# Kernel optimization log

Measured on AMD Instinct MI355X. Metric: run time of the kernel, lower is better.

The kernel has to match this reference:

```python
import jax, jax.numpy as jnp
import numpy as np

N_NODES = 25000
N_EDGES = 400000
N_GRAPHS = 1000
HID = 185
IN_CH = 9
EPS = 1e-5  # BatchNorm eps (eval mode: uses running stats)


def setup_inputs() -> dict:
    key = jax.random.key(0)
    ks = jax.random.split(key, 12)
    x = jax.random.normal(ks[0], (N_NODES, IN_CH), jnp.float32)
    edge_index = jax.random.randint(ks[1], (2, N_EDGES), 0, N_NODES, jnp.int32)
    batch = jnp.sort(jax.random.randint(ks[2], (N_NODES,), 0, N_GRAPHS, jnp.int32))
    W0 = jax.random.normal(ks[3], (IN_CH, HID), jnp.float32) * 0.3
    b0 = jnp.zeros((HID,), jnp.float32)
    W_h = jax.random.normal(ks[4], (3, HID, HID), jnp.float32) * 0.07
    b_h = jnp.zeros((3, HID), jnp.float32)
    bn_gamma = 1.0 + 0.1 * jax.random.normal(ks[5], (4, HID), jnp.float32)
    bn_beta = 0.1 * jax.random.normal(ks[6], (4, HID), jnp.float32)
    bn_mean = 0.1 * jax.random.normal(ks[7], (4, HID), jnp.float32)
    bn_var = jax.random.uniform(ks[8], (4, HID), jnp.float32, 0.5, 1.5)
    W_jk = jax.random.normal(ks[9], (4 * HID, HID), jnp.float32) * 0.05
    b_jk = jnp.zeros((HID,), jnp.float32)
    W_out = jax.random.normal(ks[10], (HID, 1), jnp.float32) * 0.1
    b_out = jnp.zeros((1,), jnp.float32)
    return dict(x=x, edge_index=edge_index, batch=batch, W0=W0, b0=b0,
                W_h=W_h, b_h=b_h, bn_gamma=bn_gamma, bn_beta=bn_beta,
                bn_mean=bn_mean, bn_var=bn_var, W_jk=W_jk, b_jk=b_jk,
                W_out=W_out, b_out=b_out)


def reference(x, edge_index, batch, W0, b0, W_h, b_h, bn_gamma, bn_beta,
              bn_mean, bn_var, W_jk, b_jk, W_out, b_out):
    N = x.shape[0]
    # GCN normalization with self-loops (gcn_norm, edge_weight = 1)
    loop = jnp.arange(N, dtype=edge_index.dtype)
    src = jnp.concatenate([edge_index[0], loop])  # [E+N]
    dst = jnp.concatenate([edge_index[1], loop])  # [E+N]
    deg = jax.ops.segment_sum(jnp.ones_like(dst, dtype=x.dtype), dst, num_segments=N)
    dis = jnp.where(deg > 0, jax.lax.rsqrt(jnp.maximum(deg, 1.0)), 0.0)
    enorm = dis[src] * dis[dst]  # [E+N]

    def gcn_conv(h, W, b):
        h = h @ W                                   # [N, HID]
        msg = h[src] * enorm[:, None]               # gather + scale, [E+N, HID]
        return jax.ops.segment_sum(msg, dst, num_segments=N) + b

    def bn_relu(h, i):
        h = (h - bn_mean[i]) * jax.lax.rsqrt(bn_var[i] + EPS) * bn_gamma[i] + bn_beta[i]
        return jax.nn.relu(h)  # dropout is identity in eval mode

    xs = []
    h = bn_relu(gcn_conv(x, W0, b0), 0)
    xs.append(h)
    for i in range(3):
        h = bn_relu(gcn_conv(h, W_h[i], b_h[i]), i + 1)
        xs.append(h)
    # JumpingKnowledge 'cat' + internal lin (740 -> 185)
    h = jnp.concatenate(xs, axis=-1) @ W_jk + b_jk  # [N, HID]
    # global_max_pool over graphs
    pooled = jax.ops.segment_max(h, batch, num_segments=N_GRAPHS)  # [G, HID]
    return pooled @ W_out + b_out  # [G, 1]
```

## Files before the change

kernel.cpp:

```cpp
#include <hip/hip_runtime.h>
#include <hip/hip_bf16.h>

#define N_NODES 25000
#define N_EDGES 400000
#define N_GRAPHS 1000
#define HID 185
#define EPS 1e-5f
#define XPITCH 768
#define APITCH 36

typedef __attribute__((ext_vector_type(8))) short bf16x8;
typedef __attribute__((ext_vector_type(4))) float f32x4;

__device__ __forceinline__ short f2bf(float f) {
    union { float f; unsigned u; } v; v.f = f;
    unsigned r = v.u + 0x7FFFu + ((v.u >> 16) & 1u);
    return (short)(r >> 16);
}
__device__ __forceinline__ float bfl(unsigned u) { return __uint_as_float(u << 16); }
__device__ __forceinline__ float bfh(unsigned u) { return __uint_as_float(u & 0xFFFF0000u); }
__device__ __forceinline__ unsigned pk2(float lo, float hi) {
    return (unsigned)(unsigned short)f2bf(lo) | ((unsigned)(unsigned short)f2bf(hi) << 16);
}

#define HW (3 * 192 * 192)
#define JW (192 * 768)
#define CNTPAD 25024
__global__ void k_setup(const float* __restrict__ W_h, const float* __restrict__ W_jk,
                        const float* __restrict__ b0, const float* __restrict__ b_h,
                        const float* __restrict__ gamma, const float* __restrict__ beta,
                        const float* __restrict__ mean, const float* __restrict__ var,
                        int* __restrict__ cnt,
                        short* __restrict__ Wt_h, short* __restrict__ Wt_jk,
                        float* __restrict__ bnsc, float* __restrict__ bnsh) {
    int idx = blockIdx.x * 256 + threadIdx.x;
    if (idx < CNTPAD) { cnt[idx] = 0; return; }
    int p = idx - CNTPAD;
    if (p < HW) {
        int l = p / (192 * 192);
        int r = p % (192 * 192);
        int n = r / 192, k = r % 192;
        float v = (n < HID && k < HID) ? W_h[(l * HID + k) * HID + n] : 0.0f;
        Wt_h[p] = f2bf(v);
    } else if (p < HW + JW) {
        int j2 = p - HW;
        int n = j2 / 768, kk = j2 % 768;
        int l = kk / 192, j = kk % 192;
        float v = (n < HID && j < HID) ? W_jk[(l * HID + j) * HID + n] : 0.0f;
        Wt_jk[j2] = f2bf(v);
    } else if (p < HW + JW + 4 * 192) {
        int li = p - HW - JW;
        int l = li / 192, c = li % 192;
        float sc = 0.0f, sh = 0.0f;
        if (c < HID) {
            float bb = (l == 0) ? b0[c] : b_h[(l - 1) * HID + c];
            sc = rsqrtf(var[l * HID + c] + EPS) * gamma[l * HID + c];
            sh = (bb - mean[l * HID + c]) * sc + beta[l * HID + c];
        }
        bnsc[li] = sc;
        bnsh[li] = sh;
    }
}

__global__ void k_deg(const int* __restrict__ dst, int* cnt, int E) {
    int i = blockIdx.x * blockDim.x + threadIdx.x;
    if (i < E) atomicAdd(&cnt[dst[i]], 1);
}

__global__ __launch_bounds__(256) void k_scan(const int* __restrict__ cnt,
                                              int* __restrict__ rowptr,
                                              float* __restrict__ dis, int N) {
    __shared__ int s[256];
    const int t = threadIdx.x;
    const int b = blockIdx.x;
    int partial = 0;
    for (int i = t; i < b * 256; i += 256) partial += cnt[i];
    s[t] = partial; __syncthreads();
    for (int off = 128; off; off >>= 1) {
        if (t < off) s[t] += s[t + off];
        __syncthreads();
    }
    const int base = s[0];
    __syncthreads();
    int i = b * 256 + t;
    int v = (i < N) ? cnt[i] : 0;
    if (i < N) dis[i] = rsqrtf((float)(v + 1));
    s[t] = v; __syncthreads();
    for (int off = 1; off < 256; off <<= 1) {
        int x2 = (t >= off) ? s[t - off] : 0;
        __syncthreads();
        s[t] += x2;
        __syncthreads();
    }
    if (i < N) rowptr[i] = base + s[t] - v;
}

__global__ void k_scatter(const int* __restrict__ src, const int* __restrict__ dst,
                          const float* __restrict__ dis,
                          int* rowptr, int2* __restrict__ csr, int E) {
    int e = blockIdx.x * blockDim.x + threadIdx.x;
    if (e < E) {
        int d = dst[e];
        int s = src[e];
        int o = atomicAdd(&rowptr[d], 1);
        csr[o] = make_int2(s, __float_as_int(dis[s]));
    }
}

__global__ void k_aggr0(const float* __restrict__ x, const float* __restrict__ dis,
                        const int* __restrict__ rowptr, const int2* __restrict__ csr,
                        float* __restrict__ xa, int N) {
    int idx = blockIdx.x * blockDim.x + threadIdx.x;
    int n = idx >> 4;
    int c = idx & 15;
    if (n >= N || c >= 9) return;
    float dn = dis[n];
    float acc = x[n * 9 + c] * dn;
    int end = rowptr[n];
    int e = n ? rowptr[n - 1] : 0;
    for (; e + 4 <= end; e += 4) {
        int2 p0 = csr[e], p1 = csr[e + 1], p2 = csr[e + 2], p3 = csr[e + 3];
        acc += x[p0.x * 9 + c] * __int_as_float(p0.y)
             + x[p1.x * 9 + c] * __int_as_float(p1.y)
             + x[p2.x * 9 + c] * __int_as_float(p2.y)
             + x[p3.x * 9 + c] * __int_as_float(p3.y);
    }
    for (; e < end; ++e) {
        int2 p = csr[e];
        acc += x[p.x * 9 + c] * __int_as_float(p.y);
    }
    xa[n * 9 + c] = acc * dn;
}

__global__ __launch_bounds__(192) void k_gemm0(const float* __restrict__ A,
                                               const float* __restrict__ W,
                                               const float* __restrict__ bnsc,
                                               const float* __restrict__ bnsh,
                                               short* __restrict__ xcat, int N) {
    __shared__ float As[8 * 9];
    const int tid = threadIdx.x;
    const int r0 = blockIdx.x * 8;
    for (int idx = tid; idx < 72; idx += 192) {
        int r = idx & 7, k = idx >> 3;
        int row = r0 + r;
        As[idx] = (row < N) ? A[row * 9 + k] : 0.0f;
    }
    __syncthreads();
    const int c = tid;
    float res[8];
    #pragma unroll
    for (int r = 0; r < 8; ++r) res[r] = 0.0f;
    if (c < HID) {
        float acc[8] = {0,0,0,0,0,0,0,0};
        for (int k = 0; k < 9; ++k) {
            float w = W[k * HID + c];
            #pragma unroll
            for (int r = 0; r < 8; ++r) acc[r] += As[k * 8 + r] * w;
        }
        float sc = bnsc[c], sh = bnsh[c];
        #pragma unroll
        for (int r = 0; r < 8; ++r)
            res[r] = fmaxf(acc[r] * sc + sh, 0.0f);
    }
    #pragma unroll
    for (int r = 0; r < 8; ++r) {
        int row = r0 + r;
        if (row < N) xcat[row * XPITCH + c] = (c < HID) ? f2bf(res[r]) : (short)0;
    }
}

__global__ __launch_bounds__(192) void k_aggr(const short* __restrict__ feat, int fpitch,
                                              const float* __restrict__ dis,
                                              const int* __restrict__ rowptr,
                                              const int2* __restrict__ csr,
                                              short* __restrict__ outp, int N) {
    const int t = threadIdx.x;
    const int n = blockIdx.x * 4 + t / 48;
    const int c0 = (t % 48) * 4;
    if (n >= N) return;
    float dn = dis[n];
    float a0, a1, a2, a3;
    {
        uint2 v = *(const uint2*)(feat + (size_t)n * fpitch + c0);
        a0 = bfl(v.x) * dn; a1 = bfh(v.x) * dn; a2 = bfl(v.y) * dn; a3 = bfh(v.y) * dn;
    }
    int end = rowptr[n];
    int e = n ? rowptr[n - 1] : 0;
    for (; e + 4 <= end; e += 4) {
        int2 p0 = csr[e], p1 = csr[e + 1], p2 = csr[e + 2], p3 = csr[e + 3];
        float w0 = __int_as_float(p0.y), w1 = __int_as_float(p1.y);
        float w2 = __int_as_float(p2.y), w3 = __int_as_float(p3.y);
        uint2 v0 = *(const uint2*)(feat + (size_t)p0.x * fpitch + c0);
        uint2 v1 = *(const uint2*)(feat + (size_t)p1.x * fpitch + c0);
        uint2 v2 = *(const uint2*)(feat + (size_t)p2.x * fpitch + c0);
        uint2 v3 = *(const uint2*)(feat + (size_t)p3.x * fpitch + c0);
        a0 += bfl(v0.x) * w0; a1 += bfh(v0.x) * w0; a2 += bfl(v0.y) * w0; a3 += bfh(v0.y) * w0;
        a0 += bfl(v1.x) * w1; a1 += bfh(v1.x) * w1; a2 += bfl(v1.y) * w1; a3 += bfh(v1.y) * w1;
        a0 += bfl(v2.x) * w2; a1 += bfh(v2.x) * w2; a2 += bfl(v2.y) * w2; a3 += bfh(v2.y) * w2;
        a0 += bfl(v3.x) * w3; a1 += bfh(v3.x) * w3; a2 += bfl(v3.y) * w3; a3 += bfh(v3.y) * w3;
    }
    for (; e < end; ++e) {
        int2 p = csr[e];
        float w = __int_as_float(p.y);
        uint2 v = *(const uint2*)(feat + (size_t)p.x * fpitch + c0);
        a0 += bfl(v.x) * w; a1 += bfh(v.x) * w; a2 += bfl(v.y) * w; a3 += bfh(v.y) * w;
    }
    uint2 p;
    p.x = pk2(a0 * dn, a1 * dn);
    p.y = pk2(a2 * dn, a3 * dn);
    *(uint2*)(outp + (size_t)n * 192 + c0) = p;
}

template<int KCH, bool BNOUT>
__global__ __launch_bounds__(256) void k_mgemm(const short* __restrict__ A, int apitch,
                                               const short* __restrict__ Bt,
                                               const float* __restrict__ bnsc,
                                               const float* __restrict__ bnsh,
                                               short* __restrict__ Cout, int cpitch, int N) {
    __shared__ short As[64 * APITCH];
    __shared__ short Bs[192 * APITCH];
    const int tid = threadIdx.x;
    const int wave = tid >> 6;
    const int lane = tid & 63;
    const int quad = lane >> 4;
    const int lm = lane & 15;
    const int r0 = blockIdx.x * 64;
    const int KTOT = KCH * 32;
    const int arow = tid >> 2, aseg = tid & 3;

    f32x4 acc[4][3];
    #pragma unroll
    for (int i = 0; i < 4; ++i)
        #pragma unroll
        for (int j = 0; j < 3; ++j) acc[i][j] = (f32x4){0.f, 0.f, 0.f, 0.f};

    for (int kc = 0; kc < KCH; ++kc) {
        const int k0 = kc * 32;
        {
            int grow = r0 + arow;
            bf16x8 v = (bf16x8){0,0,0,0,0,0,0,0};
            if (grow < N) v = *(const bf16x8*)(A + (size_t)grow * apitch + k0 + aseg * 8);
            *(bf16x8*)(As + arow * APITCH + aseg * 8) = v;
        }
        #pragma unroll
        for (int i = 0; i < 3; ++i) {
            int u = tid + i * 256;
            int n = u >> 2, seg = u & 3;
            bf16x8 v = *(const bf16x8*)(Bt + n * KTOT + k0 + seg * 8);
            *(bf16x8*)(Bs + n * APITCH + seg * 8) = v;
        }
        __syncthreads();
        bf16x8 a[4], b[3];
        #pragma unroll
        for (int mt = 0; mt < 4; ++mt)
            a[mt] = *(const bf16x8*)(As + (mt * 16 + lm) * APITCH + quad * 8);
        #pragma unroll
        for (int nt = 0; nt < 3; ++nt)
            b[nt] = *(const bf16x8*)(Bs + (wave * 48 + nt * 16 + lm) * APITCH + quad * 8);
        #pragma unroll
        for (int mt = 0; mt < 4; ++mt)
            #pragma unroll
            for (int nt = 0; nt < 3; ++nt)
                acc[mt][nt] = __builtin_amdgcn_mfma_f32_16x16x32_bf16(a[mt], b[nt], acc[mt][nt], 0, 0, 0);
        __syncthreads();
    }
    #pragma unroll
    for (int nt = 0; nt < 3; ++nt) {
        int col = wave * 48 + nt * 16 + lm;
        float sc = 1.0f, sh = 0.0f;
        if (BNOUT) { sc = bnsc[col]; sh = bnsh[col]; }
        #pragma unroll
        for (int mt = 0; mt < 4; ++mt) {
            #pragma unroll
            for (int r = 0; r < 4; ++r) {
                int row = r0 + mt * 16 + quad * 4 + r;
                if (row < N) {
                    float v = acc[mt][nt][r];
                    if (BNOUT) v = fmaxf(v * sc + sh, 0.0f);
                    Cout[(size_t)row * cpitch + col] = f2bf(v);
                }
            }
        }
    }
}

__global__ __launch_bounds__(192) void k_pool_out(const short* __restrict__ jk,
                                                  const int* __restrict__ batch,
                                                  const float* __restrict__ b_jk,
                                                  const float* __restrict__ W_out,
                                                  const float* __restrict__ b_out,
                                                  float* __restrict__ out, int N) {
    __shared__ int bounds[2];
    __shared__ float partial[3];
    const int g = blockIdx.x;
    const int tid = threadIdx.x;
    if (tid < 2) {
        int key = g + tid;
        int lo = 0, hi = N;
        while (lo < hi) {
            int mid = (lo + hi) >> 1;
            if (batch[mid] < key) lo = mid + 1; else hi = mid;
        }
        bounds[tid] = lo;
    }
    __syncthreads();
    const int beg = bounds[0], end = bounds[1];
    float mx = -3.4e38f;
    for (int n = beg; n < end; ++n)
        mx = fmaxf(mx, bfl((unsigned)(unsigned short)jk[(size_t)n * 192 + tid]));
    float p = (tid < HID) ? (mx + b_jk[tid]) * W_out[tid] : 0.0f;
    #pragma unroll
    for (int off = 32; off; off >>= 1) p += __shfl_down(p, off);
    if ((tid & 63) == 0) partial[tid >> 6] = p;
    __syncthreads();
    if (tid == 0) out[g] = partial[0] + partial[1] + partial[2] + b_out[0];
}

extern "C" void kernel_launch(void* const* d_in, const int* in_sizes, int n_in,
                              void* d_out, int out_size, void* d_ws, size_t ws_size,
                              hipStream_t stream) {
    const float* x      = (const float*)d_in[0];
    const int*   ei     = (const int*)  d_in[1];
    const int*   batch  = (const int*)  d_in[2];
    const float* W0     = (const float*)d_in[3];
    const float* b0     = (const float*)d_in[4];
    const float* W_h    = (const float*)d_in[5];
    const float* b_h    = (const float*)d_in[6];
    const float* gamma  = (const float*)d_in[7];
    const float* beta   = (const float*)d_in[8];
    const float* mean   = (const float*)d_in[9];
    const float* var    = (const float*)d_in[10];
    const float* W_jk   = (const float*)d_in[11];
    const float* b_jk   = (const float*)d_in[12];
    const float* W_out  = (const float*)d_in[13];
    const float* b_out  = (const float*)d_in[14];
    float* out = (float*)d_out;

    const int N = N_NODES, E = N_EDGES, G = N_GRAPHS;
    const int NB = (N + 255) / 256;

    float* dis   = (float*)d_ws;
    float* xa    = dis + 25024;
    float* bnsc  = xa + 225024;
    float* bnsh  = bnsc + 768;
    int2*  csr   = (int2*)(bnsh + 768);
    short* xcat  = (short*)(csr + 400000);
    short* tmp16 = xcat + 19200000;
    short* Wt_h  = tmp16 + 4800000;
    short* Wt_jk = Wt_h + 110592;
    int* rowptr  = (int*)(Wt_jk + 147456);
    int* cnt     = rowptr + 25024;

    const int* src = ei;
    const int* dst = ei + E;

    k_setup<<<(CNTPAD + HW + JW + 4 * 192 + 255) / 256, 256, 0, stream>>>(
        W_h, W_jk, b0, b_h, gamma, beta, mean, var, cnt, Wt_h, Wt_jk, bnsc, bnsh);
    k_deg<<<(E + 255) / 256, 256, 0, stream>>>(dst, cnt, E);
    k_scan<<<NB, 256, 0, stream>>>(cnt, rowptr, dis, N);
    k_scatter<<<(E + 255) / 256, 256, 0, stream>>>(src, dst, dis, rowptr, csr, E);

    k_aggr0<<<(N * 16 + 255) / 256, 256, 0, stream>>>(x, dis, rowptr, csr, xa, N);
    k_gemm0<<<(N + 7) / 8, 192, 0, stream>>>(xa, W0, bnsc, bnsh, xcat, N);

    const int MB = (N + 63) / 64;
    for (int l = 1; l < 4; ++l) {
        k_aggr<<<(N + 3) / 4, 192, 0, stream>>>(xcat + (l - 1) * 192, XPITCH,
                                                dis, rowptr, csr, tmp16, N);
        k_mgemm<6, true><<<MB, 256, 0, stream>>>(tmp16, 192,
                                                 Wt_h + (l - 1) * 192 * 192,
                                                 bnsc + l * 192, bnsh + l * 192,
                                                 xcat + l * 192, XPITCH, N);
    }

    k_mgemm<24, false><<<MB, 256, 0, stream>>>(xcat, XPITCH, Wt_jk,
                                               nullptr, nullptr, tmp16, 192, N);

    k_pool_out<<<G, 192, 0, stream>>>(tmp16, batch, b_jk, W_out, b_out, out, N);
}
```

Measured before the change: 313.8 us.

## Fuse neighbor aggregation into hidden-layer GEMM kernel via shared-memory A tile

Replaces the separate aggregation kernel and BN-fused GEMM for the three hidden layers with one kernel that gathers neighbor features for a 64-row tile directly into shared memory, then runs the MFMA GEMM with BN+ReLU epilogue. This removes the intermediate tmp16 round trip through global memory and one launch per layer. In exchange, each thread now handles a whole node's 48 columns with 48 float accumulators, so the gather is less parallel (64 rows per 256-thread block, 391 blocks) and register pressure rises, which can reduce latency hiding for the irregular gathers.

```diff
diff --git a/kernel.cpp b/kernel.cpp
--- a/kernel.cpp
+++ b/kernel.cpp
@@ -169,53 +169,115 @@
     }
 }
 
-__global__ __launch_bounds__(192) void k_aggr(const short* __restrict__ feat, int fpitch,
-                                              const float* __restrict__ dis,
-                                              const int* __restrict__ rowptr,
-                                              const int2* __restrict__ csr,
-                                              short* __restrict__ outp, int N) {
-    const int t = threadIdx.x;
-    const int n = blockIdx.x * 4 + t / 48;
-    const int c0 = (t % 48) * 4;
-    if (n >= N) return;
-    float dn = dis[n];
-    float a0, a1, a2, a3;
-    {
-        uint2 v = *(const uint2*)(feat + (size_t)n * fpitch + c0);
-        a0 = bfl(v.x) * dn; a1 = bfh(v.x) * dn; a2 = bfl(v.y) * dn; a3 = bfh(v.y) * dn;
-    }
-    int end = rowptr[n];
-    int e = n ? rowptr[n - 1] : 0;
-    for (; e + 4 <= end; e += 4) {
-        int2 p0 = csr[e], p1 = csr[e + 1], p2 = csr[e + 2], p3 = csr[e + 3];
-        float w0 = __int_as_float(p0.y), w1 = __int_as_float(p1.y);
-        float w2 = __int_as_float(p2.y), w3 = __int_as_float(p3.y);
-        uint2 v0 = *(const uint2*)(feat + (size_t)p0.x * fpitch + c0);
-        uint2 v1 = *(const uint2*)(feat + (size_t)p1.x * fpitch + c0);
-        uint2 v2 = *(const uint2*)(feat + (size_t)p2.x * fpitch + c0);
-        uint2 v3 = *(const uint2*)(feat + (size_t)p3.x * fpitch + c0);
-        a0 += bfl(v0.x) * w0; a1 += bfh(v0.x) * w0; a2 += bfl(v0.y) * w0; a3 += bfh(v0.y) * w0;
-        a0 += bfl(v1.x) * w1; a1 += bfh(v1.x) * w1; a2 += bfl(v1.y) * w1; a3 += bfh(v1.y) * w1;
-        a0 += bfl(v2.x) * w2; a1 += bfh(v2.x) * w2; a2 += bfl(v2.y) * w2; a3 += bfh(v2.y) * w2;
-        a0 += bfl(v3.x) * w3; a1 += bfh(v3.x) * w3; a2 += bfl(v3.y) * w3; a3 += bfh(v3.y) * w3;
-    }
-    for (; e < end; ++e) {
-        int2 p = csr[e];
-        float w = __int_as_float(p.y);
-        uint2 v = *(const uint2*)(feat + (size_t)p.x * fpitch + c0);
-        a0 += bfl(v.x) * w; a1 += bfh(v.x) * w; a2 += bfl(v.y) * w; a3 += bfh(v.y) * w;
-    }
-    uint2 p;
-    p.x = pk2(a0 * dn, a1 * dn);
-    p.y = pk2(a2 * dn, a3 * dn);
-    *(uint2*)(outp + (size_t)n * 192 + c0) = p;
-}
-
-template<int KCH, bool BNOUT>
-__global__ __launch_bounds__(256) void k_mgemm(const short* __restrict__ A, int apitch,
+__global__ __launch_bounds__(256) void k_layer(const short* __restrict__ feat,
+                                               const float* __restrict__ dis,
+                                               const int* __restrict__ rowptr,
+                                               const int2* __restrict__ csr,
                                                const short* __restrict__ Bt,
                                                const float* __restrict__ bnsc,
                                                const float* __restrict__ bnsh,
+                                               short* __restrict__ outp, int N) {
+    __shared__ short As[6 * 64 * APITCH];
+    __shared__ short Bs[192 * APITCH];
+    const int tid = threadIdx.x;
+    const int r0 = blockIdx.x * 64;
+
+    {
+        const int r = tid >> 2;
+        const int c0 = (tid & 3) * 48;
+        const int n = r0 + r;
+        float a[48];
+        if (n < N) {
+            float dn = dis[n];
+            const short* fr = feat + (size_t)n * XPITCH + c0;
+            #pragma unroll
+            for (int i = 0; i < 12; ++i) {
+                uint2 v = *(const uint2*)(fr + i * 4);
+                a[i*4+0] = bfl(v.x) * dn; a[i*4+1] = bfh(v.x) * dn;
+                a[i*4+2] = bfl(v.y) * dn; a[i*4+3] = bfh(v.y) * dn;
+            }
+            int end = rowptr[n];
+            int e = n ? rowptr[n - 1] : 0;
+            for (; e < end; ++e) {
+                int2 p = csr[e];
+                float w = __int_as_float(p.y);
+                const short* fs = feat + (size_t)p.x * XPITCH + c0;
+                #pragma unroll
+                for (int i = 0; i < 12; ++i) {
+                    uint2 v = *(const uint2*)(fs + i * 4);
+                    a[i*4+0] += bfl(v.x) * w; a[i*4+1] += bfh(v.x) * w;
+                    a[i*4+2] += bfl(v.y) * w; a[i*4+3] += bfh(v.y) * w;
+                }
+            }
+            #pragma unroll
+            for (int i = 0; i < 48; ++i) a[i] *= dn;
+        } else {
+            #pragma unroll
+            for (int i = 0; i < 48; ++i) a[i] = 0.0f;
+        }
+        #pragma unroll
+        for (int i = 0; i < 24; ++i) {
+            int c = c0 + 2 * i;
+            int kc = c >> 5, off = c & 31;
+            *(unsigned*)(As + kc * 64 * APITCH + r * APITCH + off) = pk2(a[2*i], a[2*i+1]);
+        }
+    }
+    __syncthreads();
+
+    const int wave = tid >> 6;
+    const int lane = tid & 63;
+    const int quad = lane >> 4;
+    const int lm = lane & 15;
+
+    f32x4 acc[4][3];
+    #pragma unroll
+    for (int i = 0; i < 4; ++i)
+        #pragma unroll
+        for (int j = 0; j < 3; ++j) acc[i][j] = (f32x4){0.f, 0.f, 0.f, 0.f};
+
+    for (int kc = 0; kc < 6; ++kc) {
+        const int k0 = kc * 32;
+        #pragma unroll
+        for (int i = 0; i < 3; ++i) {
+            int u = tid + i * 256;
+            int nb = u >> 2, seg = u & 3;
+            bf16x8 v = *(const bf16x8*)(Bt + nb * 192 + k0 + seg * 8);
+            *(bf16x8*)(Bs + nb * APITCH + seg * 8) = v;
+        }
+        __syncthreads();
+        bf16x8 a[4], b[3];
+        #pragma unroll
+        for (int mt = 0; mt < 4; ++mt)
+            a[mt] = *(const bf16x8*)(As + kc * 64 * APITCH + (mt * 16 + lm) * APITCH + quad * 8);
+        #pragma unroll
+        for (int nt = 0; nt < 3; ++nt)
+            b[nt] = *(const bf16x8*)(Bs + (wave * 48 + nt * 16 + lm) * APITCH + quad * 8);
+        #pragma unroll
+        for (int mt = 0; mt < 4; ++mt)
+            #pragma unroll
+            for (int nt = 0; nt < 3; ++nt)
+                acc[mt][nt] = __builtin_amdgcn_mfma_f32_16x16x32_bf16(a[mt], b[nt], acc[mt][nt], 0, 0, 0);
+        __syncthreads();
+    }
+    #pragma unroll
+    for (int nt = 0; nt < 3; ++nt) {
+        int col = wave * 48 + nt * 16 + lm;
+        float sc = bnsc[col], sh = bnsh[col];
+        #pragma unroll
+        for (int mt = 0; mt < 4; ++mt) {
+            #pragma unroll
+            for (int r = 0; r < 4; ++r) {
+                int row = r0 + mt * 16 + quad * 4 + r;
+                if (row < N)
+                    outp[(size_t)row * XPITCH + col] = f2bf(fmaxf(acc[mt][nt][r] * sc + sh, 0.0f));
+            }
+        }
+    }
+}
+
+template<int KCH>
+__global__ __launch_bounds__(256) void k_mgemm(const short* __restrict__ A, int apitch,
+                                               const short* __restrict__ Bt,
                                                short* __restrict__ Cout, int cpitch, int N) {
     __shared__ short As[64 * APITCH];
     __shared__ short Bs[192 * APITCH];
@@ -267,18 +329,12 @@
     #pragma unroll
     for (int nt = 0; nt < 3; ++nt) {
         int col = wave * 48 + nt * 16 + lm;
-        float sc = 1.0f, sh = 0.0f;
-        if (BNOUT) { sc = bnsc[col]; sh = bnsh[col]; }
         #pragma unroll
         for (int mt = 0; mt < 4; ++mt) {
             #pragma unroll
             for (int r = 0; r < 4; ++r) {
                 int row = r0 + mt * 16 + quad * 4 + r;
-                if (row < N) {
-                    float v = acc[mt][nt][r];
-                    if (BNOUT) v = fmaxf(v * sc + sh, 0.0f);
-                    Cout[(size_t)row * cpitch + col] = f2bf(v);
-                }
+                if (row < N) Cout[(size_t)row * cpitch + col] = f2bf(acc[mt][nt][r]);
             }
         }
     }
@@ -365,16 +421,13 @@
 
     const int MB = (N + 63) / 64;
     for (int l = 1; l < 4; ++l) {
-        k_aggr<<<(N + 3) / 4, 192, 0, stream>>>(xcat + (l - 1) * 192, XPITCH,
-                                                dis, rowptr, csr, tmp16, N);
-        k_mgemm<6, true><<<MB, 256, 0, stream>>>(tmp16, 192,
-                                                 Wt_h + (l - 1) * 192 * 192,
-                                                 bnsc + l * 192, bnsh + l * 192,
-                                                 xcat + l * 192, XPITCH, N);
-    }
-
-    k_mgemm<24, false><<<MB, 256, 0, stream>>>(xcat, XPITCH, Wt_jk,
-                                               nullptr, nullptr, tmp16, 192, N);
+        k_layer<<<MB, 256, 0, stream>>>(xcat + (l - 1) * 192, dis, rowptr, csr,
+                                        Wt_h + (l - 1) * 192 * 192,
+                                        bnsc + l * 192, bnsh + l * 192,
+                                        xcat + l * 192, N);
+    }
+
+    k_mgemm<24><<<MB, 256, 0, stream>>>(xcat, XPITCH, Wt_jk, tmp16, 192, N);
 
     k_pool_out<<<G, 192, 0, stream>>>(tmp16, batch, b_jk, W_out, b_out, out, N);
 }
```

New measurement: 314.7 us. About the same (+0.3%).
